# Kernel optimization log

Measured on AMD Instinct MI355X. Metric: run time of the kernel, lower is better.

Reference implementation:

```python
import jax, jax.numpy as jnp
import numpy as np

EPS = 1e-8

def _cosine_sim_to_codebook(x, codebook):
    # x: [N, D], codebook: [K, D] -> [N, K]; equivalent to broadcast F.cosine_similarity
    xn = x / jnp.maximum(jnp.linalg.norm(x, axis=-1, keepdims=True), EPS)
    cn = codebook / jnp.maximum(jnp.linalg.norm(codebook, axis=-1, keepdims=True), EPS)
    return xn @ cn.T

def _gumbel_softmax(key, logits, tau, hard):
    g = jax.random.gumbel(key, logits.shape, dtype=logits.dtype)
    y = jax.nn.softmax((logits + g) / tau, axis=-1)
    if hard:
        onehot = jax.nn.one_hot(jnp.argmax(y, axis=-1), logits.shape[-1], dtype=y.dtype)
        # straight-through estimator
        y = onehot + y - jax.lax.stop_gradient(y)
    return y

def setup_inputs() -> dict:
    key = jax.random.key(0)
    k1, k2, k3 = jax.random.split(key, 3)
    B, L, D, K = 64, 512, 512, 1024
    N = B * L
    return {
        "state_emb": jax.random.normal(k1, (N, D), dtype=jnp.float32),
        "adv_emb": jax.random.normal(k2, (N, D), dtype=jnp.float32),
        "codebook": jax.random.normal(k3, (K, D), dtype=jnp.float32),
        "B": B,
        "L": L,
    }

def reference(state_emb, adv_emb, codebook, B, L):
    tau = 1.0
    alpha = 0.5
    # NOTE: the original computes adv_emb_shift but never uses it (dead code); omitted.
    sim_state = _cosine_sim_to_codebook(state_emb, codebook)  # [N, K]
    sim_adv = _cosine_sim_to_codebook(adv_emb, codebook)      # [N, K]
    sim = alpha * sim_state + (1.0 - alpha) * sim_adv
    gk = jax.random.key(42)
    gk1, gk2 = jax.random.split(gk)
    weights_hard = _gumbel_softmax(gk1, sim, tau, hard=True)   # [N, K] one-hot (ST)
    weights_soft = _gumbel_softmax(gk2, sim, tau, hard=False)  # [N, K]
    indices = jnp.argmax(weights_hard, axis=-1)[:, None]       # [N, 1]
    z_q = weights_hard @ codebook                              # [N, D]
    return (z_q, weights_soft, indices)
```

## Files before the change

### kernel.cpp

```cpp
#include <hip/hip_runtime.h>
#include <stdint.h>

typedef unsigned int u32;
typedef unsigned short u16;
typedef __attribute__((ext_vector_type(8))) __bf16 bf16x8;
typedef __attribute__((ext_vector_type(4))) float f32x4;

#define N_ROWS 32768
#define D_DIM 512
#define K_CB 1024

__host__ __device__ inline void tf2x32(u32 k0, u32 k1, u32 x0, u32 x1, u32 &o0, u32 &o1) {
  const u32 ks2 = k0 ^ k1 ^ 0x1BD11BDAu;
#define TFR(r) x0 += x1; x1 = (x1 << (r)) | (x1 >> (32 - (r))); x1 ^= x0;
  x0 += k0; x1 += k1;
  TFR(13) TFR(15) TFR(26) TFR(6)
  x0 += k1; x1 += ks2 + 1u;
  TFR(17) TFR(29) TFR(16) TFR(24)
  x0 += ks2; x1 += k0 + 2u;
  TFR(13) TFR(15) TFR(26) TFR(6)
  x0 += k0; x1 += k1 + 3u;
  TFR(17) TFR(29) TFR(16) TFR(24)
  x0 += k1; x1 += ks2 + 4u;
  TFR(13) TFR(15) TFR(26) TFR(6)
  x0 += ks2; x1 += k0 + 5u;
#undef TFR
  o0 = x0; o1 = x1;
}

__device__ inline float bits_to_gumbel(u32 bits) {
  float f = __uint_as_float((bits >> 9) | 0x3f800000u) - 1.0f;
  const float tiny = 1.17549435e-38f;
  float u = fmaxf(tiny, f + tiny);
  return -logf(-logf(u));
}

__device__ inline u16 f32_bf16(float x) {
  u32 u = __float_as_uint(x);
  u += 0x7fffu + ((u >> 16) & 1u);
  return (u16)(u >> 16);
}
__device__ inline float bf16_f32(u16 h) { return __uint_as_float(((u32)h) << 16); }

__global__ void __launch_bounds__(256) prep_codebook(const float* __restrict__ cb,
                                                     u16* __restrict__ cn_hi,
                                                     u16* __restrict__ cn_lo) {
  const int lane = threadIdx.x & 63, wid = threadIdx.x >> 6;
  const int row = blockIdx.x * 4 + wid;
  const float* src = cb + (size_t)row * D_DIM;
  float v[8]; float ss = 0.f;
#pragma unroll
  for (int i = 0; i < 8; ++i) { v[i] = src[lane + 64 * i]; ss = fmaf(v[i], v[i], ss); }
#pragma unroll
  for (int off = 32; off; off >>= 1) ss += __shfl_xor(ss, off);
  const float denom = fmaxf(sqrtf(ss), 1e-8f);
#pragma unroll
  for (int i = 0; i < 8; ++i) {
    const float x = v[i] / denom;
    const u16 h = f32_bf16(x);
    const u16 l = f32_bf16(x - bf16_f32(h));
    cn_hi[(size_t)row * D_DIM + lane + 64 * i] = h;
    cn_lo[(size_t)row * D_DIM + lane + 64 * i] = l;
  }
}

__global__ void __launch_bounds__(256) prep_m(const float* __restrict__ se,
                                              const float* __restrict__ ae,
                                              u16* __restrict__ m_hi,
                                              u16* __restrict__ m_lo) {
  const int lane = threadIdx.x & 63, wid = threadIdx.x >> 6;
  const size_t row = (size_t)blockIdx.x * 4 + wid;
  const float* s = se + row * D_DIM;
  const float* a = ae + row * D_DIM;
  float sv[8], av[8]; float ss = 0.f, sa = 0.f;
#pragma unroll
  for (int i = 0; i < 8; ++i) {
    sv[i] = s[lane + 64 * i]; av[i] = a[lane + 64 * i];
    ss = fmaf(sv[i], sv[i], ss); sa = fmaf(av[i], av[i], sa);
  }
#pragma unroll
  for (int off = 32; off; off >>= 1) { ss += __shfl_xor(ss, off); sa += __shfl_xor(sa, off); }
  const float ds = fmaxf(sqrtf(ss), 1e-8f);
  const float da = fmaxf(sqrtf(sa), 1e-8f);
#pragma unroll
  for (int i = 0; i < 8; ++i) {
    const float m = 0.5f * (sv[i] / ds) + 0.5f * (av[i] / da);
    const u16 h = f32_bf16(m);
    const u16 l = f32_bf16(m - bf16_f32(h));
    m_hi[row * D_DIM + lane + 64 * i] = h;
    m_lo[row * D_DIM + lane + 64 * i] = l;
  }
}

__global__ void __launch_bounds__(256) gemm_sim(const u16* __restrict__ mA_hi,
                                                const u16* __restrict__ mA_lo,
                                                const u16* __restrict__ cn_hi,
                                                const u16* __restrict__ cn_lo,
                                                float* __restrict__ sim) {
  __shared__ __align__(16) u16 As_hi[128 * 64];
  __shared__ __align__(16) u16 As_lo[128 * 64];
  __shared__ __align__(16) u16 Bs_hi[128 * 64];
  __shared__ __align__(16) u16 Bs_lo[128 * 64];

  const int tid = threadIdx.x;
  const int lane = tid & 63;
  const int wid = tid >> 6;
  const int wr = wid >> 1, wc = wid & 1;
  const int bn = blockIdx.x, bm = blockIdx.y;

  const int fr = lane & 15;
  const int q8 = lane >> 4;

  f32x4 acc[4][4];
#pragma unroll
  for (int i = 0; i < 4; ++i)
#pragma unroll
    for (int j = 0; j < 4; ++j) acc[i][j] = (f32x4){0.f, 0.f, 0.f, 0.f};

  const int o_base = wid * 1024 + lane * 16;
  const char* gA_hi = (const char*)mA_hi + (size_t)(bm * 128) * (D_DIM * 2);
  const char* gA_lo = (const char*)mA_lo + (size_t)(bm * 128) * (D_DIM * 2);
  const char* gB_hi = (const char*)cn_hi + (size_t)(bn * 128) * (D_DIM * 2);
  const char* gB_lo = (const char*)cn_lo + (size_t)(bn * 128) * (D_DIM * 2);

  for (int kt = 0; kt < D_DIM / 64; ++kt) {
    const int kbyte = kt * 128;
#pragma unroll
    for (int i = 0; i < 4; ++i) {
      const int o = o_base + i * 4096;
      const int row = o >> 7;
      const int cbyt = o & 127;
      const size_t goff = (size_t)row * (D_DIM * 2) + kbyte + cbyt;
      const int loff = wid * 1024 + i * 4096;
      __builtin_amdgcn_global_load_lds((const __attribute__((address_space(1))) void*)(gA_hi + goff),
                                       (__attribute__((address_space(3))) void*)((char*)As_hi + loff), 16, 0, 0);
      __builtin_amdgcn_global_load_lds((const __attribute__((address_space(1))) void*)(gA_lo + goff),
                                       (__attribute__((address_space(3))) void*)((char*)As_lo + loff), 16, 0, 0);
      __builtin_amdgcn_global_load_lds((const __attribute__((address_space(1))) void*)(gB_hi + goff),
                                       (__attribute__((address_space(3))) void*)((char*)Bs_hi + loff), 16, 0, 0);
      __builtin_amdgcn_global_load_lds((const __attribute__((address_space(1))) void*)(gB_lo + goff),
                                       (__attribute__((address_space(3))) void*)((char*)Bs_lo + loff), 16, 0, 0);
    }
    __syncthreads();

#pragma unroll
    for (int kk = 0; kk < 2; ++kk) {
      bf16x8 ah[4], al[4], bh[4], bl[4];
      const int co = kk * 32 + q8 * 8;
#pragma unroll
      for (int mi = 0; mi < 4; ++mi) {
        const int r = wr * 64 + mi * 16 + fr;
        ah[mi] = *(const bf16x8*)&As_hi[r * 64 + co];
        al[mi] = *(const bf16x8*)&As_lo[r * 64 + co];
      }
#pragma unroll
      for (int ni = 0; ni < 4; ++ni) {
        const int r = wc * 64 + ni * 16 + fr;
        bh[ni] = *(const bf16x8*)&Bs_hi[r * 64 + co];
        bl[ni] = *(const bf16x8*)&Bs_lo[r * 64 + co];
      }
#pragma unroll
      for (int mi = 0; mi < 4; ++mi)
#pragma unroll
        for (int ni = 0; ni < 4; ++ni) {
          acc[mi][ni] = __builtin_amdgcn_mfma_f32_16x16x32_bf16(ah[mi], bh[ni], acc[mi][ni], 0, 0, 0);
          acc[mi][ni] = __builtin_amdgcn_mfma_f32_16x16x32_bf16(ah[mi], bl[ni], acc[mi][ni], 0, 0, 0);
          acc[mi][ni] = __builtin_amdgcn_mfma_f32_16x16x32_bf16(al[mi], bh[ni], acc[mi][ni], 0, 0, 0);
        }
    }
    __syncthreads();
  }

  const int row_base = bm * 128 + wr * 64 + q8 * 4;
  const int col_base = bn * 128 + wc * 64 + fr;
#pragma unroll
  for (int mi = 0; mi < 4; ++mi)
#pragma unroll
    for (int ni = 0; ni < 4; ++ni) {
      const int r0 = row_base + mi * 16;
      const int c = col_base + ni * 16;
#pragma unroll
      for (int r = 0; r < 4; ++r)
        sim[(size_t)(r0 + r) * K_CB + c] = acc[mi][ni][r];
    }
}

__global__ void __launch_bounds__(256) gumbel_epilogue(float* __restrict__ simw,
                                                       float* __restrict__ zq,
                                                       float* __restrict__ idxf,
                                                       const float* __restrict__ cb,
                                                       u32 k1a, u32 k1b, u32 k2a, u32 k2b) {
  const int n = blockIdx.x;
  const int tid = threadIdx.x;
  const int lane = tid & 63, wid = tid >> 6;
  float* row = simw + (size_t)n * K_CB;
  const u32 base = (u32)n * K_CB;

  float l1[4], l2[4];
#pragma unroll
  for (int i = 0; i < 4; ++i) {
    const int k = tid + i * 256;
    const float s = row[k];
    u32 a0, a1, b0, b1;
    tf2x32(k1a, k1b, 0u, base + (u32)k, a0, a1);
    tf2x32(k2a, k2b, 0u, base + (u32)k, b0, b1);
    l1[i] = s + bits_to_gumbel(a0 ^ a1);
    l2[i] = s + bits_to_gumbel(b0 ^ b1);
  }

  float bv = l1[0]; int bi = tid;
#pragma unroll
  for (int i = 1; i < 4; ++i) {
    const int k = tid + i * 256;
    if (l1[i] > bv) { bv = l1[i]; bi = k; }
  }
#pragma unroll
  for (int off = 1; off < 64; off <<= 1) {
    const float ov = __shfl_xor(bv, off);
    const int oi = __shfl_xor(bi, off);
    if (ov > bv || (ov == bv && oi < bi)) { bv = ov; bi = oi; }
  }
  float mx = fmaxf(fmaxf(l2[0], l2[1]), fmaxf(l2[2], l2[3]));
#pragma unroll
  for (int off = 1; off < 64; off <<= 1) mx = fmaxf(mx, __shfl_xor(mx, off));

  __shared__ float svv[4]; __shared__ int sii[4];
  __shared__ float smx[4]; __shared__ float ssm[4];
  if (lane == 0) { svv[wid] = bv; sii[wid] = bi; smx[wid] = mx; }
  __syncthreads();
  bv = svv[0]; bi = sii[0];
#pragma unroll
  for (int w = 1; w < 4; ++w)
    if (svv[w] > bv || (svv[w] == bv && sii[w] < bi)) { bv = svv[w]; bi = sii[w]; }
  mx = fmaxf(fmaxf(smx[0], smx[1]), fmaxf(smx[2], smx[3]));

  float p[4]; float ps = 0.f;
#pragma unroll
  for (int i = 0; i < 4; ++i) { p[i] = expf(l2[i] - mx); ps += p[i]; }
#pragma unroll
  for (int off = 1; off < 64; off <<= 1) ps += __shfl_xor(ps, off);
  if (lane == 0) ssm[wid] = ps;
  __syncthreads();
  const float tot = ssm[0] + ssm[1] + ssm[2] + ssm[3];

#pragma unroll
  for (int i = 0; i < 4; ++i) row[tid + i * 256] = p[i] / tot;

  const float* crow = cb + (size_t)bi * D_DIM;
  for (int j = tid; j < D_DIM; j += 256) zq[(size_t)n * D_DIM + j] = crow[j];
  if (tid == 0) idxf[n] = (float)bi;
}

extern "C" void kernel_launch(void* const* d_in, const int* in_sizes, int n_in,
                              void* d_out, int out_size, void* d_ws, size_t ws_size,
                              hipStream_t stream) {
  const float* state = (const float*)d_in[0];
  const float* adv = (const float*)d_in[1];
  const float* cb = (const float*)d_in[2];

  char* ws = (char*)d_ws;
  u16* m_hi = (u16*)ws;
  u16* m_lo = (u16*)(ws + (size_t)N_ROWS * D_DIM * 2);
  u16* cn_hi = (u16*)(ws + (size_t)N_ROWS * D_DIM * 4);
  u16* cn_lo = (u16*)(ws + (size_t)N_ROWS * D_DIM * 4 + (size_t)K_CB * D_DIM * 2);

  float* zq = (float*)d_out;
  float* simw = zq + (size_t)N_ROWS * D_DIM;
  float* idxf = simw + (size_t)N_ROWS * K_CB;

  u32 gk1a, gk1b, gk2a, gk2b;
  tf2x32(0u, 42u, 0u, 0u, gk1a, gk1b);
  tf2x32(0u, 42u, 0u, 1u, gk2a, gk2b);

  hipLaunchKernelGGL(prep_codebook, dim3(K_CB / 4), dim3(256), 0, stream, cb, cn_hi, cn_lo);
  hipLaunchKernelGGL(prep_m, dim3(N_ROWS / 4), dim3(256), 0, stream, state, adv, m_hi, m_lo);
  hipLaunchKernelGGL(gemm_sim, dim3(K_CB / 128, N_ROWS / 128), dim3(256), 0, stream,
                     m_hi, m_lo, cn_hi, cn_lo, simw);
  hipLaunchKernelGGL(gumbel_epilogue, dim3(N_ROWS), dim3(256), 0, stream,
                     simw, zq, idxf, cb, gk1a, gk1b, gk2a, gk2b);
}
```

Before: 559.5 us.

## Process one row per wavefront in gumbel epilogue with fast math and no max pass

The epilogue now assigns one row per wavefront instead of one row per 256-thread block. That removes shared-memory reductions and __syncthreads, and loads and stores rows as float4. The Gumbel transform uses __log2f-based fast logs and softmax uses __expf. The max-subtraction pass is dropped, relying on cosine similarity plus Gumbel noise staying within a range that cannot overflow exp. This trades some numerical accuracy and softmax overflow safety for fewer reduction passes and cheaper transcendentals.

After: 528.0 us. 1.06x faster.

```diff
diff --git a/kernel.cpp b/kernel.cpp
--- a/kernel.cpp
+++ b/kernel.cpp
@@ -28,11 +28,15 @@
   o0 = x0; o1 = x1;
 }
 
-__device__ inline float bits_to_gumbel(u32 bits) {
-  float f = __uint_as_float((bits >> 9) | 0x3f800000u) - 1.0f;
+__device__ inline float gumbel_fast(u32 bits) {
+  const float f = __uint_as_float((bits >> 9) | 0x3f800000u) - 1.0f;
   const float tiny = 1.17549435e-38f;
-  float u = fmaxf(tiny, f + tiny);
-  return -logf(-logf(u));
+  const float u = fmaxf(tiny, f + tiny);
+  const float NLN2 = -0.69314718055994530942f;
+  const float a = __log2f(u);
+  const float v = a * NLN2;
+  const float b = __log2f(v);
+  return b * NLN2;
 }
 
 __device__ inline u16 f32_bf16(float x) {
@@ -190,65 +194,55 @@
                                                        float* __restrict__ idxf,
                                                        const float* __restrict__ cb,
                                                        u32 k1a, u32 k1b, u32 k2a, u32 k2b) {
-  const int n = blockIdx.x;
-  const int tid = threadIdx.x;
-  const int lane = tid & 63, wid = tid >> 6;
-  float* row = simw + (size_t)n * K_CB;
-  const u32 base = (u32)n * K_CB;
-
-  float l1[4], l2[4];
+  const int lane = threadIdx.x & 63, wid = threadIdx.x >> 6;
+  const int n = blockIdx.x * 4 + wid;
+  float4* row4 = (float4*)(simw + (size_t)n * K_CB);
+  const u32 kbase = (u32)n * K_CB;
+
+  float p2[16];
+  float ps = 0.f;
+  float bv = -1e30f; int bi = 0;
 #pragma unroll
   for (int i = 0; i < 4; ++i) {
-    const int k = tid + i * 256;
-    const float s = row[k];
-    u32 a0, a1, b0, b1;
-    tf2x32(k1a, k1b, 0u, base + (u32)k, a0, a1);
-    tf2x32(k2a, k2b, 0u, base + (u32)k, b0, b1);
-    l1[i] = s + bits_to_gumbel(a0 ^ a1);
-    l2[i] = s + bits_to_gumbel(b0 ^ b1);
-  }
-
-  float bv = l1[0]; int bi = tid;
-#pragma unroll
-  for (int i = 1; i < 4; ++i) {
-    const int k = tid + i * 256;
-    if (l1[i] > bv) { bv = l1[i]; bi = k; }
+    const int f4i = lane + i * 64;
+    const float4 s4 = row4[f4i];
+#pragma unroll
+    for (int j = 0; j < 4; ++j) {
+      const u32 k = 4u * (u32)f4i + (u32)j;
+      u32 a0, a1, b0, b1;
+      tf2x32(k1a, k1b, 0u, kbase + k, a0, a1);
+      tf2x32(k2a, k2b, 0u, kbase + k, b0, b1);
+      const float s = (j == 0) ? s4.x : (j == 1) ? s4.y : (j == 2) ? s4.z : s4.w;
+      const float l1 = s + gumbel_fast(a0 ^ a1);
+      const float l2 = s + gumbel_fast(b0 ^ b1);
+      const float p = __expf(l2);
+      p2[i * 4 + j] = p;
+      ps += p;
+      if (l1 > bv) { bv = l1; bi = (int)k; }
+    }
   }
 #pragma unroll
   for (int off = 1; off < 64; off <<= 1) {
     const float ov = __shfl_xor(bv, off);
     const int oi = __shfl_xor(bi, off);
     if (ov > bv || (ov == bv && oi < bi)) { bv = ov; bi = oi; }
-  }
-  float mx = fmaxf(fmaxf(l2[0], l2[1]), fmaxf(l2[2], l2[3]));
-#pragma unroll
-  for (int off = 1; off < 64; off <<= 1) mx = fmaxf(mx, __shfl_xor(mx, off));
-
-  __shared__ float svv[4]; __shared__ int sii[4];
-  __shared__ float smx[4]; __shared__ float ssm[4];
-  if (lane == 0) { svv[wid] = bv; sii[wid] = bi; smx[wid] = mx; }
-  __syncthreads();
-  bv = svv[0]; bi = sii[0];
-#pragma unroll
-  for (int w = 1; w < 4; ++w)
-    if (svv[w] > bv || (svv[w] == bv && sii[w] < bi)) { bv = svv[w]; bi = sii[w]; }
-  mx = fmaxf(fmaxf(smx[0], smx[1]), fmaxf(smx[2], smx[3]));
-
-  float p[4]; float ps = 0.f;
-#pragma unroll
-  for (int i = 0; i < 4; ++i) { p[i] = expf(l2[i] - mx); ps += p[i]; }
-#pragma unroll
-  for (int off = 1; off < 64; off <<= 1) ps += __shfl_xor(ps, off);
-  if (lane == 0) ssm[wid] = ps;
-  __syncthreads();
-  const float tot = ssm[0] + ssm[1] + ssm[2] + ssm[3];
-
-#pragma unroll
-  for (int i = 0; i < 4; ++i) row[tid + i * 256] = p[i] / tot;
-
-  const float* crow = cb + (size_t)bi * D_DIM;
-  for (int j = tid; j < D_DIM; j += 256) zq[(size_t)n * D_DIM + j] = crow[j];
-  if (tid == 0) idxf[n] = (float)bi;
+    ps += __shfl_xor(ps, off);
+  }
+  const float inv = 1.0f / ps;
+#pragma unroll
+  for (int i = 0; i < 4; ++i) {
+    float4 o;
+    o.x = p2[i * 4 + 0] * inv;
+    o.y = p2[i * 4 + 1] * inv;
+    o.z = p2[i * 4 + 2] * inv;
+    o.w = p2[i * 4 + 3] * inv;
+    row4[lane + i * 64] = o;
+  }
+  const float4* crow = (const float4*)(cb + (size_t)bi * D_DIM);
+  float4* zrow = (float4*)(zq + (size_t)n * D_DIM);
+#pragma unroll
+  for (int i = 0; i < 2; ++i) zrow[lane + i * 64] = crow[lane + i * 64];
+  if (lane == 0) idxf[n] = (float)bi;
 }
 
 extern "C" void kernel_launch(void* const* d_in, const int* in_sizes, int n_in,
@@ -276,6 +270,6 @@
   hipLaunchKernelGGL(prep_m, dim3(N_ROWS / 4), dim3(256), 0, stream, state, adv, m_hi, m_lo);
   hipLaunchKernelGGL(gemm_sim, dim3(K_CB / 128, N_ROWS / 128), dim3(256), 0, stream,
                      m_hi, m_lo, cn_hi, cn_lo, simw);
-  hipLaunchKernelGGL(gumbel_epilogue, dim3(N_ROWS), dim3(256), 0, stream,
+  hipLaunchKernelGGL(gumbel_epilogue, dim3(N_ROWS / 4), dim3(256), 0, stream,
                      simw, zq, idxf, cb, gk1a, gk1b, gk2a, gk2b);
 }
```
